# Kernel tuning notes

Measured on AMD Instinct MI355X. Metric: run time of the kernel, lower is better.

## Reference

```python
import jax, jax.numpy as jnp
import numpy as np
import math

B, H, S, D = 8, 16, 256, 256  # S == D is required by the module's math

def setup_inputs() -> dict:
    key = jax.random.key(0)
    kq, kk, kv, km = jax.random.split(key, 4)
    q = jax.random.normal(kq, (B, H, S, D), dtype=jnp.float32)
    k = jax.random.normal(kk, (B, H, S, D), dtype=jnp.float32)
    v = jax.random.normal(kv, (B, H, S, D), dtype=jnp.float32)
    u = jax.random.uniform(km, (1, H, S, S), dtype=jnp.float32)
    # additive mask: large negative where 'masked', 0.0 elsewhere
    mask = jnp.where(u > 0.7, jnp.float32(-1000.0), jnp.float32(0.0))
    return {"q": q, "k": k, "v": v, "mask": mask}

def reference(q, k, v, mask):
    scale = 1.0 / math.sqrt(q.shape[-1])
    # qk: [B,H,S,S]
    qk = jnp.einsum('bhsd,bhtd->bhst', q, k) * scale + mask
    # first matmul with v: [B,H,S,D] (D == S)
    attn = jnp.einsum('bhst,bhtd->bhsd', qk, v)
    # masked_fill where additive mask == 0.0 (broadcasts [1,H,S,S] -> [B,H,S,D])
    attn = jnp.where(mask == 0.0, jnp.float32(-1e9), attn)
    attn = jax.nn.softmax(attn.astype(jnp.float32), axis=-1).astype(q.dtype)
    # second matmul with v: [B,H,S,D]
    out = jnp.einsum('bhst,bhtd->bhsd', attn, v)
    return out
```

## Files before the change

kernel.cpp:

```cpp
#include <hip/hip_runtime.h>
#include <math.h>

namespace {
constexpr int S  = 256;
constexpr int NT = 256;
constexpr float SCALE = 0.0625f;
constexpr int KLD = 264;
}

typedef __bf16 bf16x4 __attribute__((ext_vector_type(4)));
typedef __bf16 bf16x8 __attribute__((ext_vector_type(8)));
typedef float  f32x4  __attribute__((ext_vector_type(4)));

#define MFMA(a, b, c) __builtin_amdgcn_mfma_f32_16x16x32_bf16((a), (b), (c), 0, 0, 0)

__global__ __launch_bounds__(NT) void vsplit_kernel(
    const float* __restrict__ v,
    __bf16* __restrict__ vth, __bf16* __restrict__ vtl, __bf16* __restrict__ vtll)
{
    __shared__ float tile[32][257];
    const int bh = blockIdx.x >> 3;
    const int tc = blockIdx.x & 7;
    const int tid = threadIdx.x;

    const float* vb = v + (size_t)bh * S * S + (size_t)tc * 32 * S;
    {
        const int c4 = (tid & 63) * 4;
        const int r  = tid >> 6;
        #pragma unroll
        for (int rr = 0; rr < 8; ++rr) {
            const int row = rr * 4 + r;
            const float4 f = *(const float4*)&vb[(size_t)row * S + c4];
            tile[row][c4 + 0] = f.x; tile[row][c4 + 1] = f.y;
            tile[row][c4 + 2] = f.z; tile[row][c4 + 3] = f.w;
        }
    }
    __syncthreads();

    const size_t obase = (size_t)bh * S * S + (size_t)tc * 8192;
    #pragma unroll
    for (int it = 0; it < 4; ++it) {
        const int id  = it * 256 + tid;
        const int j   = id >> 6;
        const int l4  = (id >> 4) & 3;
        const int l15 = id & 15;
        const int d   = j * 16 + l15;
        const int t0  = l4 * 8;
        bf16x8 hv, lv, llv;
        #pragma unroll
        for (int e = 0; e < 8; ++e) {
            const float x = tile[t0 + e][d];
            const __bf16 hi = (__bf16)x;
            const float  hf = (float)hi;
            const __bf16 lo = (__bf16)(x - hf);
            const float  lf = (float)lo;
            hv[e] = hi; lv[e] = lo; llv[e] = (__bf16)(x - hf - lf);
        }
        const size_t oi = obase + (size_t)id * 8;
        *(bf16x8*)&vth[oi]  = hv;
        *(bf16x8*)&vtl[oi]  = lv;
        *(bf16x8*)&vtll[oi] = llv;
    }
}

__global__ __launch_bounds__(NT, 2) void qkt_kernel(
    const float* __restrict__ q, const float* __restrict__ k,
    __bf16* __restrict__ r_hi, __bf16* __restrict__ r_lo, int swz)
{
    __shared__ __align__(16) __bf16 kh[64 * KLD];
    __shared__ __align__(16) __bf16 kl[64 * KLD];

    const int tid = threadIdx.x;
    const int w = tid >> 6, l = tid & 63, l15 = l & 15, l4 = l >> 4;

    int L = blockIdx.x;
    if (swz) L = (blockIdx.x & 7) * ((int)gridDim.x >> 3) + (blockIdx.x >> 3);
    const int bh = L >> 4;
    const int s0 = ((L >> 2) & 3) << 6;
    const int t0 = (L & 3) << 6;

    const float* qb = q + ((size_t)bh << 16);
    const float* kb = k + ((size_t)bh << 16);

    {
        const float* ksrc = kb + (size_t)t0 * S;
        #pragma unroll 4
        for (int it = 0; it < 16; ++it) {
            const int idx = it * 1024 + tid * 4;
            const float4 f = *(const float4*)&ksrc[idx];
            const float xs[4] = {f.x, f.y, f.z, f.w};
            bf16x4 hv, lv;
            #pragma unroll
            for (int e = 0; e < 4; ++e) {
                const __bf16 hi = (__bf16)xs[e];
                hv[e] = hi; lv[e] = (__bf16)(xs[e] - (float)hi);
            }
            const int row = idx >> 8;
            const int col = idx & 255;
            *(bf16x4*)&kh[row * KLD + col] = hv;
            *(bf16x4*)&kl[row * KLD + col] = lv;
        }
    }

    bf16x8 qh[8], ql[8];
    {
        const float* qr = qb + (size_t)(s0 + 16 * w + l15) * S;
        #pragma unroll
        for (int kc = 0; kc < 8; ++kc) {
            const float4 f0 = *(const float4*)&qr[kc * 32 + l4 * 8];
            const float4 f1 = *(const float4*)&qr[kc * 32 + l4 * 8 + 4];
            const float xs[8] = {f0.x, f0.y, f0.z, f0.w, f1.x, f1.y, f1.z, f1.w};
            bf16x8 hv, lv;
            #pragma unroll
            for (int e = 0; e < 8; ++e) {
                const float x = xs[e] * SCALE;
                const __bf16 hi = (__bf16)x;
                hv[e] = hi; lv[e] = (__bf16)(x - (float)hi);
            }
            qh[kc] = hv; ql[kc] = lv;
        }
    }
    __syncthreads();

    f32x4 acc[4];
    #pragma unroll
    for (int j = 0; j < 4; ++j) acc[j] = (f32x4){0.f, 0.f, 0.f, 0.f};

    #pragma unroll
    for (int kc = 0; kc < 8; ++kc) {
        #pragma unroll
        for (int j = 0; j < 4; ++j) {
            const int bo = (j * 16 + l15) * KLD + kc * 32 + l4 * 8;
            const bf16x8 khf = *(const bf16x8*)&kh[bo];
            const bf16x8 klf = *(const bf16x8*)&kl[bo];
            acc[j] = MFMA(qh[kc], khf, acc[j]);
            acc[j] = MFMA(qh[kc], klf, acc[j]);
            acc[j] = MFMA(ql[kc], khf, acc[j]);
        }
    }

    __bf16* rh_b = r_hi + ((size_t)bh << 16);
    __bf16* rl_b = r_lo + ((size_t)bh << 16);
    #pragma unroll
    for (int j = 0; j < 4; ++j) {
        #pragma unroll
        for (int rr = 0; rr < 4; ++rr) {
            const int row = s0 + 16 * w + l4 * 4 + rr;
            const int t   = t0 + j * 16 + l15;
            const float rv = acc[j][rr];
            const __bf16 hi = (__bf16)rv;
            rh_b[(size_t)row * S + t] = hi;
            rl_b[(size_t)row * S + t] = (__bf16)(rv - (float)hi);
        }
    }
}

#define SRC_OF(sp) ((sp) == 0 ? vth : (sp) == 1 ? vtl : vtll)

#define P2_LOAD(tc)                                                           \
    _Pragma("unroll")                                                         \
    for (int r_ = 0; r_ < 12; ++r_) {                                         \
        const int sp_ = r_ >> 2, qt_ = r_ & 3;                                \
        const __bf16* s_ = SRC_OF(sp_);                                       \
        stg[r_] = *(const bf16x8*)&s_[hb + (size_t)(tc) * 8192 + qt_ * 2048 + tid * 8]; \
    }

#define P2_WRITE()                                                            \
    _Pragma("unroll")                                                         \
    for (int r_ = 0; r_ < 12; ++r_) {                                         \
        const int sp_ = r_ >> 2, qt_ = r_ & 3;                                \
        *(bf16x8*)&arena[sp_ * 8192 + qt_ * 2048 + tid * 8] = stg[r_];        \
    }

#define P3_LOAD(tc)                                                           \
    _Pragma("unroll")                                                         \
    for (int r_ = 0; r_ < 8; ++r_) {                                          \
        const int sp_ = r_ >> 2, qt_ = r_ & 3;                                \
        const __bf16* s_ = SRC_OF(sp_);                                       \
        stg[r_] = *(const bf16x8*)&s_[hb + (size_t)(tc) * 8192 + qt_ * 2048 + tid * 8]; \
    }

#define P3_WRITE()                                                            \
    _Pragma("unroll")                                                         \
    for (int r_ = 0; r_ < 8; ++r_) {                                          \
        const int sp_ = r_ >> 2, qt_ = r_ & 3;                                \
        *(bf16x8*)&arena[16384 + sp_ * 8192 + qt_ * 2048 + tid * 8] = stg[r_];\
    }

__global__ __launch_bounds__(NT, 2) void attn2_kernel(
    const float* __restrict__ mask,
    const __bf16* __restrict__ r_hi, const __bf16* __restrict__ r_lo,
    const __bf16* __restrict__ vth, const __bf16* __restrict__ vtl,
    const __bf16* __restrict__ vtll,
    float* __restrict__ out, int H, int swz)
{
    __shared__ __align__(16) __bf16 arena[32768];

    const int tid = threadIdx.x;
    const int w = tid >> 6, l = tid & 63, l15 = l & 15, l4 = l >> 4;

    int L = blockIdx.x;
    if (swz) L = (blockIdx.x & 7) * ((int)gridDim.x >> 3) + (blockIdx.x >> 3);
    const int bh = L >> 2;
    const int s0 = (L & 3) << 6;
    const int h  = bh % H;

    const size_t hb = (size_t)bh << 16;
    const float* mbase = mask + ((size_t)h << 16);

    const int arow_g = s0 + 16 * w + l15;
    const __bf16* rh_p = r_hi + hb + (size_t)arow_g * S;
    const __bf16* rl_p = r_lo + hb + (size_t)arow_g * S;
    const float*  m_p  = mbase + (size_t)arow_g * S;

    bf16x8 stg[12];

    f32x4 acc2[16];
    #pragma unroll
    for (int j = 0; j < 16; ++j) acc2[j] = (f32x4){0.f, 0.f, 0.f, 0.f};

    P2_LOAD(0);
    P2_WRITE();
    P2_LOAD(1);
    bf16x8 rhc, rlc; float4 m0c, m1c;
    {
        const int ko_ = l4 * 8;
        rhc = *(const bf16x8*)&rh_p[ko_];
        rlc = *(const bf16x8*)&rl_p[ko_];
        m0c = *(const float4*)&m_p[ko_];
        m1c = *(const float4*)&m_p[ko_ + 4];
    }
    __syncthreads();

    #pragma unroll
    for (int tc = 0; tc < 8; ++tc) {
        bf16x8 rhn, rln; float4 m0n, m1n;
        if (tc < 7) {
            const int ko_ = (tc + 1) * 32 + l4 * 8;
            rhn = *(const bf16x8*)&rh_p[ko_];
            rln = *(const bf16x8*)&rl_p[ko_];
            m0n = *(const float4*)&m_p[ko_];
            m1n = *(const float4*)&m_p[ko_ + 4];
        }
        bf16x8 mf;
        mf[0] = (__bf16)m0c.x; mf[1] = (__bf16)m0c.y;
        mf[2] = (__bf16)m0c.z; mf[3] = (__bf16)m0c.w;
        mf[4] = (__bf16)m1c.x; mf[5] = (__bf16)m1c.y;
        mf[6] = (__bf16)m1c.z; mf[7] = (__bf16)m1c.w;

        #pragma unroll
        for (int j = 0; j < 16; ++j) {
            const int fo = j * 512 + l * 8;
            const bf16x8 vh  = *(const bf16x8*)&arena[fo];
            const bf16x8 vl  = *(const bf16x8*)&arena[8192 + fo];
            const bf16x8 vll = *(const bf16x8*)&arena[16384 + fo];
            acc2[j] = MFMA(mf,  vh,  acc2[j]);
            acc2[j] = MFMA(mf,  vl,  acc2[j]);
            acc2[j] = MFMA(mf,  vll, acc2[j]);
            acc2[j] = MFMA(rhc, vh,  acc2[j]);
            acc2[j] = MFMA(rhc, vl,  acc2[j]);
            acc2[j] = MFMA(rlc, vh,  acc2[j]);
        }
        __syncthreads();
        if (tc < 7) {
            P2_WRITE();
            if (tc < 6) P2_LOAD(tc + 2);
            rhc = rhn; rlc = rln; m0c = m0n; m1c = m1n;
            __syncthreads();
        }
    }

    P3_LOAD(0);

    #pragma unroll
    for (int rr = 0; rr < 4; ++rr) {
        const int srow = 16 * w + l4 * 4 + rr;
        const float* mrow = mbase + (size_t)(s0 + srow) * S;
        float mx = -3.4e38f;
        #pragma unroll
        for (int j = 0; j < 16; ++j) {
            const float mval = mrow[j * 16 + l15];
            const float a = (mval == 0.0f) ? -1e9f : acc2[j][rr];
            acc2[j][rr] = a;
            mx = fmaxf(mx, a);
        }
        #pragma unroll
        for (int off = 1; off < 16; off <<= 1)
            mx = fmaxf(mx, __shfl_xor(mx, off, 64));
        float sm = 0.f;
        #pragma unroll
        for (int j = 0; j < 16; ++j) {
            const float e = __expf(acc2[j][rr] - mx);
            acc2[j][rr] = e;
            sm += e;
        }
        #pragma unroll
        for (int off = 1; off < 16; off <<= 1)
            sm += __shfl_xor(sm, off, 64);
        const float inv = 1.0f / sm;
        #pragma unroll
        for (int j = 0; j < 16; ++j) {
            const int t = j * 16 + l15;
            arena[((srow << 8) + t) ^ ((srow & 7) << 3)] = (__bf16)(acc2[j][rr] * inv);
        }
    }
    P3_WRITE();
    P3_LOAD(1);
    __syncthreads();

    f32x4 acc3[16];
    #pragma unroll
    for (int j = 0; j < 16; ++j) acc3[j] = (f32x4){0.f, 0.f, 0.f, 0.f};

    const int prow = 16 * w + l15;
    #pragma unroll
    for (int tc = 0; tc < 8; ++tc) {
        const int pb = ((prow << 8) + tc * 32 + l4 * 8) ^ ((prow & 7) << 3);
        const bf16x8 pa = *(const bf16x8*)&arena[pb];
        #pragma unroll
        for (int j = 0; j < 16; ++j) {
            const int fo = 16384 + j * 512 + l * 8;
            acc3[j] = MFMA(pa, *(const bf16x8*)&arena[fo], acc3[j]);
            acc3[j] = MFMA(pa, *(const bf16x8*)&arena[8192 + fo], acc3[j]);
        }
        __syncthreads();
        if (tc < 7) {
            P3_WRITE();
            if (tc < 6) P3_LOAD(tc + 2);
            __syncthreads();
        }
    }

    float* ob = out + hb + (size_t)s0 * S;
    #pragma unroll
    for (int j = 0; j < 16; ++j) {
        #pragma unroll
        for (int rr = 0; rr < 4; ++rr)
            ob[(size_t)(16 * w + l4 * 4 + rr) * S + j * 16 + l15] = acc3[j][rr];
    }
}

__global__ __launch_bounds__(NT) void transpose_k_kernel(
    const float* __restrict__ k, float* __restrict__ kt)
{
    __shared__ float tile[64][65];
    const int tileIdx = blockIdx.x & 15;
    const int bh      = blockIdx.x >> 4;
    const int ti = (tileIdx >> 2) * 64;
    const int tj = (tileIdx & 3) * 64;
    const float* kb = k  + (size_t)bh * S * S;
    float*      ktb = kt + (size_t)bh * S * S;
    const int c  = threadIdx.x & 63;
    const int r4 = threadIdx.x >> 6;
    #pragma unroll
    for (int rr = 0; rr < 64; rr += 4)
        tile[rr + r4][c] = kb[(size_t)(ti + rr + r4) * S + tj + c];
    __syncthreads();
    #pragma unroll
    for (int rr = 0; rr < 64; rr += 4)
        ktb[(size_t)(tj + rr + r4) * S + ti + c] = tile[c][rr + r4];
}

template <int RPB>
__global__ __launch_bounds__(NT) void fused_attn_rpb(
    const float* __restrict__ q, const float* __restrict__ kt,
    const float* __restrict__ v, const float* __restrict__ mask,
    float* __restrict__ out, int nbh, int H, int swizzle)
{
    __shared__ float qT[S][RPB];
    __shared__ float sT[S][RPB];
    __shared__ float redbuf[4][RPB];

    const int tid = threadIdx.x;
    constexpr int NRB = S / RPB;
    int bh, rb;
    if (swizzle) {
        const int xcd  = blockIdx.x & 7;
        const int slot = blockIdx.x >> 3;
        const int hpx  = nbh >> 3;
        bh = xcd * hpx + (slot % hpx);
        rb = slot / hpx;
    } else {
        bh = blockIdx.x / NRB;
        rb = blockIdx.x % NRB;
    }
    const int h  = bh % H;
    const int s0 = rb * RPB;

    const float* qb  = q    + (size_t)bh * S * S;
    const float* ktb = kt   + (size_t)bh * S * S;
    const float* vb  = v    + (size_t)bh * S * S;
    const float* mb  = mask + (size_t)h  * S * S + (size_t)s0 * S;
    float*       ob  = out  + (size_t)bh * S * S + (size_t)s0 * S;

    #pragma unroll
    for (int si = 0; si < RPB; ++si)
        qT[tid][si] = qb[(size_t)(s0 + si) * S + tid];
    __syncthreads();

    {
        float acc[RPB];
        #pragma unroll
        for (int si = 0; si < RPB; ++si) acc[si] = 0.f;
        #pragma unroll 4
        for (int i = 0; i < S; ++i) {
            const float kv = ktb[(size_t)i * S + tid];
            #pragma unroll
            for (int si4 = 0; si4 < RPB; si4 += 4) {
                const float4 qa = *reinterpret_cast<const float4*>(&qT[i][si4]);
                acc[si4+0] = fmaf(qa.x, kv, acc[si4+0]);
                acc[si4+1] = fmaf(qa.y, kv, acc[si4+1]);
                acc[si4+2] = fmaf(qa.z, kv, acc[si4+2]);
                acc[si4+3] = fmaf(qa.w, kv, acc[si4+3]);
            }
        }
        #pragma unroll
        for (int si4 = 0; si4 < RPB; si4 += 4) {
            float4 t4;
            t4.x = fmaf(acc[si4+0], SCALE, mb[(size_t)(si4+0)*S + tid]);
            t4.y = fmaf(acc[si4+1], SCALE, mb[(size_t)(si4+1)*S + tid]);
            t4.z = fmaf(acc[si4+2], SCALE, mb[(size_t)(si4+2)*S + tid]);
            t4.w = fmaf(acc[si4+3], SCALE, mb[(size_t)(si4+3)*S + tid]);
            *reinterpret_cast<float4*>(&sT[tid][si4]) = t4;
        }
    }
    __syncthreads();

    float a1[RPB];
    #pragma unroll
    for (int si = 0; si < RPB; ++si) a1[si] = 0.f;
    #pragma unroll 2
    for (int t = 0; t < S; ++t) {
        const float vv = vb[(size_t)t * S + tid];
        #pragma unroll
        for (int si4 = 0; si4 < RPB; si4 += 4) {
            const float4 pa = *reinterpret_cast<const float4*>(&sT[t][si4]);
            a1[si4+0] = fmaf(pa.x, vv, a1[si4+0]);
            a1[si4+1] = fmaf(pa.y, vv, a1[si4+1]);
            a1[si4+2] = fmaf(pa.z, vv, a1[si4+2]);
            a1[si4+3] = fmaf(pa.w, vv, a1[si4+3]);
        }
    }
    #pragma unroll
    for (int si = 0; si < RPB; ++si)
        if (mb[(size_t)si * S + tid] == 0.0f) a1[si] = -1e9f;

    const int lane = tid & 63;
    const int wv   = tid >> 6;
    #pragma unroll
    for (int si = 0; si < RPB; ++si) {
        float m = a1[si];
        #pragma unroll
        for (int off = 32; off > 0; off >>= 1)
            m = fmaxf(m, __shfl_down(m, off, 64));
        if (lane == 0) redbuf[wv][si] = m;
    }
    __syncthreads();
    float e[RPB];
    #pragma unroll
    for (int si = 0; si < RPB; ++si) {
        const float m = fmaxf(fmaxf(redbuf[0][si], redbuf[1][si]),
                              fmaxf(redbuf[2][si], redbuf[3][si]));
        e[si] = __expf(a1[si] - m);
    }
    __syncthreads();
    #pragma unroll
    for (int si = 0; si < RPB; ++si) {
        float sm = e[si];
        #pragma unroll
        for (int off = 32; off > 0; off >>= 1)
            sm += __shfl_down(sm, off, 64);
        if (lane == 0) redbuf[wv][si] = sm;
    }
    __syncthreads();
    #pragma unroll
    for (int si4 = 0; si4 < RPB; si4 += 4) {
        float4 t4;
        #pragma unroll
        for (int jj = 0; jj < 4; ++jj) {
            const int si = si4 + jj;
            const float sm = redbuf[0][si] + redbuf[1][si] +
                             redbuf[2][si] + redbuf[3][si];
            (&t4.x)[jj] = e[si] / sm;
        }
        *reinterpret_cast<float4*>(&sT[tid][si4]) = t4;
    }
    __syncthreads();

    float o[RPB];
    #pragma unroll
    for (int si = 0; si < RPB; ++si) o[si] = 0.f;
    #pragma unroll 2
    for (int t = 0; t < S; ++t) {
        const float vv = vb[(size_t)t * S + tid];
        #pragma unroll
        for (int si4 = 0; si4 < RPB; si4 += 4) {
            const float4 pa = *reinterpret_cast<const float4*>(&sT[t][si4]);
            o[si4+0] = fmaf(pa.x, vv, o[si4+0]);
            o[si4+1] = fmaf(pa.y, vv, o[si4+1]);
            o[si4+2] = fmaf(pa.z, vv, o[si4+2]);
            o[si4+3] = fmaf(pa.w, vv, o[si4+3]);
        }
    }
    #pragma unroll
    for (int si = 0; si < RPB; ++si)
        ob[(size_t)si * S + tid] = o[si];
}

extern "C" void kernel_launch(void* const* d_in, const int* in_sizes, int n_in,
                              void* d_out, int out_size, void* d_ws, size_t ws_size,
                              hipStream_t stream) {
    const float* q    = (const float*)d_in[0];
    const float* k    = (const float*)d_in[1];
    const float* v    = (const float*)d_in[2];
    const float* mask = (const float*)d_in[3];
    float* out = (float*)d_out;

    const int nbh = in_sizes[0] / (S * S);
    const int H   = in_sizes[3] / (S * S);
    const size_t he = (size_t)nbh * S * S;
    const size_t need = he * sizeof(__bf16) * 5;
    const size_t kt_bytes = he * sizeof(float);

    if (ws_size >= need) {
        __bf16* vth  = (__bf16*)d_ws;
        __bf16* vtl  = vth + he;
        __bf16* vtll = vtl + he;
        __bf16* rhi  = vtll + he;
        __bf16* rlo  = rhi + he;
        const int nblk_q = nbh * 16;
        const int nblk_a = nbh * 4;
        const int swzq = (nblk_q % 8 == 0) ? 1 : 0;
        const int swza = (nblk_a % 8 == 0) ? 1 : 0;
        vsplit_kernel<<<dim3(nbh * 8), NT, 0, stream>>>(v, vth, vtl, vtll);
        qkt_kernel<<<dim3(nblk_q), NT, 0, stream>>>(q, k, rhi, rlo, swzq);
        attn2_kernel<<<dim3(nblk_a), NT, 0, stream>>>(
            mask, rhi, rlo, vth, vtl, vtll, out, H, swza);
    } else if (ws_size >= kt_bytes) {
        float* kt = (float*)d_ws;
        transpose_k_kernel<<<dim3(nbh * 16), NT, 0, stream>>>(k, kt);
        constexpr int RPB = 16;
        const int grid = nbh * (S / RPB);
        const int swz = (nbh % 8 == 0) ? 1 : 0;
        fused_attn_rpb<RPB><<<dim3(grid), NT, 0, stream>>>(
            q, kt, v, mask, out, nbh, H, swz);
    }
}
```

Measured before the change: 91.85 us.

## Merge V split and QK^T kernels into one launch; raise MFMA wave priority

The separate V-splitting kernel and QK^T kernel are combined into a single prep kernel whose blocks take one of three roles (two QK^T tiles, one V split tile) and share one LDS arena. This removes a kernel launch and the serialization gap between two independent passes, letting them overlap on the GPU. Separately, s_setprio is raised around the MFMA inner loops in the attention kernel to favour matrix issue over other waves. The merged kernel uses the larger LDS footprint for all blocks, which may reduce occupancy for the V role.

```diff
diff --git a/kernel.cpp b/kernel.cpp
--- a/kernel.cpp
+++ b/kernel.cpp
@@ -14,143 +14,152 @@
 
 #define MFMA(a, b, c) __builtin_amdgcn_mfma_f32_16x16x32_bf16((a), (b), (c), 0, 0, 0)
 
-__global__ __launch_bounds__(NT) void vsplit_kernel(
+__global__ __launch_bounds__(NT, 2) void prep_kernel(
+    const float* __restrict__ q, const float* __restrict__ k,
     const float* __restrict__ v,
-    __bf16* __restrict__ vth, __bf16* __restrict__ vtl, __bf16* __restrict__ vtll)
+    __bf16* __restrict__ vth, __bf16* __restrict__ vtl, __bf16* __restrict__ vtll,
+    __bf16* __restrict__ r_hi, __bf16* __restrict__ r_lo,
+    int nbh, int swzq)
 {
-    __shared__ float tile[32][257];
-    const int bh = blockIdx.x >> 3;
-    const int tc = blockIdx.x & 7;
-    const int tid = threadIdx.x;
-
-    const float* vb = v + (size_t)bh * S * S + (size_t)tc * 32 * S;
-    {
-        const int c4 = (tid & 63) * 4;
-        const int r  = tid >> 6;
-        #pragma unroll
-        for (int rr = 0; rr < 8; ++rr) {
-            const int row = rr * 4 + r;
-            const float4 f = *(const float4*)&vb[(size_t)row * S + c4];
-            tile[row][c4 + 0] = f.x; tile[row][c4 + 1] = f.y;
-            tile[row][c4 + 2] = f.z; tile[row][c4 + 3] = f.w;
-        }
-    }
-    __syncthreads();
-
-    const size_t obase = (size_t)bh * S * S + (size_t)tc * 8192;
-    #pragma unroll
-    for (int it = 0; it < 4; ++it) {
-        const int id  = it * 256 + tid;
-        const int j   = id >> 6;
-        const int l4  = (id >> 4) & 3;
-        const int l15 = id & 15;
-        const int d   = j * 16 + l15;
-        const int t0  = l4 * 8;
-        bf16x8 hv, lv, llv;
-        #pragma unroll
-        for (int e = 0; e < 8; ++e) {
-            const float x = tile[t0 + e][d];
-            const __bf16 hi = (__bf16)x;
-            const float  hf = (float)hi;
-            const __bf16 lo = (__bf16)(x - hf);
-            const float  lf = (float)lo;
-            hv[e] = hi; lv[e] = lo; llv[e] = (__bf16)(x - hf - lf);
-        }
-        const size_t oi = obase + (size_t)id * 8;
-        *(bf16x8*)&vth[oi]  = hv;
-        *(bf16x8*)&vtl[oi]  = lv;
-        *(bf16x8*)&vtll[oi] = llv;
-    }
-}
-
-__global__ __launch_bounds__(NT, 2) void qkt_kernel(
-    const float* __restrict__ q, const float* __restrict__ k,
-    __bf16* __restrict__ r_hi, __bf16* __restrict__ r_lo, int swz)
-{
-    __shared__ __align__(16) __bf16 kh[64 * KLD];
-    __shared__ __align__(16) __bf16 kl[64 * KLD];
-
-    const int tid = threadIdx.x;
-    const int w = tid >> 6, l = tid & 63, l15 = l & 15, l4 = l >> 4;
-
-    int L = blockIdx.x;
-    if (swz) L = (blockIdx.x & 7) * ((int)gridDim.x >> 3) + (blockIdx.x >> 3);
-    const int bh = L >> 4;
-    const int s0 = ((L >> 2) & 3) << 6;
-    const int t0 = (L & 3) << 6;
-
-    const float* qb = q + ((size_t)bh << 16);
-    const float* kb = k + ((size_t)bh << 16);
-
-    {
-        const float* ksrc = kb + (size_t)t0 * S;
-        #pragma unroll 4
-        for (int it = 0; it < 16; ++it) {
-            const int idx = it * 1024 + tid * 4;
-            const float4 f = *(const float4*)&ksrc[idx];
-            const float xs[4] = {f.x, f.y, f.z, f.w};
-            bf16x4 hv, lv;
+    __shared__ __align__(16) unsigned char lds_arena[64 * KLD * 2 * 2];
+
+    const int tid  = threadIdx.x;
+    const int trio = blockIdx.x / 3;
+    const int role = blockIdx.x % 3;
+
+    if (role < 2) {
+        __bf16* kh = (__bf16*)lds_arena;
+        __bf16* kl = kh + 64 * KLD;
+
+        const int w = tid >> 6, l = tid & 63, l15 = l & 15, l4 = l >> 4;
+
+        int L = trio * 2 + role;
+        if (swzq) {
+            const int n = nbh * 16;
+            L = (L & 7) * (n >> 3) + (L >> 3);
+        }
+        const int bh = L >> 4;
+        const int s0 = ((L >> 2) & 3) << 6;
+        const int t0 = (L & 3) << 6;
+
+        const float* qb = q + ((size_t)bh << 16);
+        const float* kb = k + ((size_t)bh << 16);
+
+        {
+            const float* ksrc = kb + (size_t)t0 * S;
+            #pragma unroll 4
+            for (int it = 0; it < 16; ++it) {
+                const int idx = it * 1024 + tid * 4;
+                const float4 f = *(const float4*)&ksrc[idx];
+                const float xs[4] = {f.x, f.y, f.z, f.w};
+                bf16x4 hv, lv;
+                #pragma unroll
+                for (int e = 0; e < 4; ++e) {
+                    const __bf16 hi = (__bf16)xs[e];
+                    hv[e] = hi; lv[e] = (__bf16)(xs[e] - (float)hi);
+                }
+                const int row = idx >> 8;
+                const int col = idx & 255;
+                *(bf16x4*)&kh[row * KLD + col] = hv;
+                *(bf16x4*)&kl[row * KLD + col] = lv;
+            }
+        }
+
+        bf16x8 qh[8], ql[8];
+        {
+            const float* qr = qb + (size_t)(s0 + 16 * w + l15) * S;
             #pragma unroll
-            for (int e = 0; e < 4; ++e) {
-                const __bf16 hi = (__bf16)xs[e];
-                hv[e] = hi; lv[e] = (__bf16)(xs[e] - (float)hi);
-            }
-            const int row = idx >> 8;
-            const int col = idx & 255;
-            *(bf16x4*)&kh[row * KLD + col] = hv;
-            *(bf16x4*)&kl[row * KLD + col] = lv;
-        }
-    }
-
-    bf16x8 qh[8], ql[8];
-    {
-        const float* qr = qb + (size_t)(s0 + 16 * w + l15) * S;
+            for (int kc = 0; kc < 8; ++kc) {
+                const float4 f0 = *(const float4*)&qr[kc * 32 + l4 * 8];
+                const float4 f1 = *(const float4*)&qr[kc * 32 + l4 * 8 + 4];
+                const float xs[8] = {f0.x, f0.y, f0.z, f0.w, f1.x, f1.y, f1.z, f1.w};
+                bf16x8 hv, lv;
+                #pragma unroll
+                for (int e = 0; e < 8; ++e) {
+                    const float x = xs[e] * SCALE;
+                    const __bf16 hi = (__bf16)x;
+                    hv[e] = hi; lv[e] = (__bf16)(x - (float)hi);
+                }
+                qh[kc] = hv; ql[kc] = lv;
+            }
+        }
+        __syncthreads();
+
+        f32x4 acc[4];
+        #pragma unroll
+        for (int j = 0; j < 4; ++j) acc[j] = (f32x4){0.f, 0.f, 0.f, 0.f};
+
         #pragma unroll
         for (int kc = 0; kc < 8; ++kc) {
-            const float4 f0 = *(const float4*)&qr[kc * 32 + l4 * 8];
-            const float4 f1 = *(const float4*)&qr[kc * 32 + l4 * 8 + 4];
-            const float xs[8] = {f0.x, f0.y, f0.z, f0.w, f1.x, f1.y, f1.z, f1.w};
-            bf16x8 hv, lv;
+            #pragma unroll
+            for (int j = 0; j < 4; ++j) {
+                const int bo = (j * 16 + l15) * KLD + kc * 32 + l4 * 8;
+                const bf16x8 khf = *(const bf16x8*)&kh[bo];
+                const bf16x8 klf = *(const bf16x8*)&kl[bo];
+                acc[j] = MFMA(qh[kc], khf, acc[j]);
+                acc[j] = MFMA(qh[kc], klf, acc[j]);
+                acc[j] = MFMA(ql[kc], khf, acc[j]);
+            }
+        }
+
+        __bf16* rh_b = r_hi + ((size_t)bh << 16);
+        __bf16* rl_b = r_lo + ((size_t)bh << 16);
+        #pragma unroll
+        for (int j = 0; j < 4; ++j) {
+            #pragma unroll
+            for (int rr = 0; rr < 4; ++rr) {
+                const int row = s0 + 16 * w + l4 * 4 + rr;
+                const int t   = t0 + j * 16 + l15;
+                const float rv = acc[j][rr];
+                const __bf16 hi = (__bf16)rv;
+                rh_b[(size_t)row * S + t] = hi;
+                rl_b[(size_t)row * S + t] = (__bf16)(rv - (float)hi);
+            }
+        }
+    } else {
+        float (*tile)[257] = (float(*)[257])lds_arena;
+
+        const int vi = trio;
+        const int bh = vi >> 3;
+        const int tc = vi & 7;
+
+        const float* vb = v + (size_t)bh * S * S + (size_t)tc * 32 * S;
+        {
+            const int c4 = (tid & 63) * 4;
+            const int r  = tid >> 6;
+            #pragma unroll
+            for (int rr = 0; rr < 8; ++rr) {
+                const int row = rr * 4 + r;
+                const float4 f = *(const float4*)&vb[(size_t)row * S + c4];
+                tile[row][c4 + 0] = f.x; tile[row][c4 + 1] = f.y;
+                tile[row][c4 + 2] = f.z; tile[row][c4 + 3] = f.w;
+            }
+        }
+        __syncthreads();
+
+        const size_t obase = (size_t)bh * S * S + (size_t)tc * 8192;
+        #pragma unroll
+        for (int it = 0; it < 4; ++it) {
+            const int id  = it * 256 + tid;
+            const int j   = id >> 6;
+            const int l4  = (id >> 4) & 3;
+            const int l15 = id & 15;
+            const int d   = j * 16 + l15;
+            const int t0  = l4 * 8;
+            bf16x8 hv, lv, llv;
             #pragma unroll
             for (int e = 0; e < 8; ++e) {
-                const float x = xs[e] * SCALE;
+                const float x = tile[t0 + e][d];
                 const __bf16 hi = (__bf16)x;
-                hv[e] = hi; lv[e] = (__bf16)(x - (float)hi);
-            }
-            qh[kc] = hv; ql[kc] = lv;
-        }
-    }
-    __syncthreads();
-
-    f32x4 acc[4];
-    #pragma unroll
-    for (int j = 0; j < 4; ++j) acc[j] = (f32x4){0.f, 0.f, 0.f, 0.f};
-
-    #pragma unroll
-    for (int kc = 0; kc < 8; ++kc) {
-        #pragma unroll
-        for (int j = 0; j < 4; ++j) {
-            const int bo = (j * 16 + l15) * KLD + kc * 32 + l4 * 8;
-            const bf16x8 khf = *(const bf16x8*)&kh[bo];
-            const bf16x8 klf = *(const bf16x8*)&kl[bo];
-            acc[j] = MFMA(qh[kc], khf, acc[j]);
-            acc[j] = MFMA(qh[kc], klf, acc[j]);
-            acc[j] = MFMA(ql[kc], khf, acc[j]);
-        }
-    }
-
-    __bf16* rh_b = r_hi + ((size_t)bh << 16);
-    __bf16* rl_b = r_lo + ((size_t)bh << 16);
-    #pragma unroll
-    for (int j = 0; j < 4; ++j) {
-        #pragma unroll
-        for (int rr = 0; rr < 4; ++rr) {
-            const int row = s0 + 16 * w + l4 * 4 + rr;
-            const int t   = t0 + j * 16 + l15;
-            const float rv = acc[j][rr];
-            const __bf16 hi = (__bf16)rv;
-            rh_b[(size_t)row * S + t] = hi;
-            rl_b[(size_t)row * S + t] = (__bf16)(rv - (float)hi);
+                const float  hf = (float)hi;
+                const __bf16 lo = (__bf16)(x - hf);
+                const float  lf = (float)lo;
+                hv[e] = hi; lv[e] = lo; llv[e] = (__bf16)(x - hf - lf);
+            }
+            const size_t oi = obase + (size_t)id * 8;
+            *(bf16x8*)&vth[oi]  = hv;
+            *(bf16x8*)&vtl[oi]  = lv;
+            *(bf16x8*)&vtll[oi] = llv;
         }
     }
 }
@@ -248,6 +257,7 @@
         mf[4] = (__bf16)m1c.x; mf[5] = (__bf16)m1c.y;
         mf[6] = (__bf16)m1c.z; mf[7] = (__bf16)m1c.w;
 
+        __builtin_amdgcn_s_setprio(1);
         #pragma unroll
         for (int j = 0; j < 16; ++j) {
             const int fo = j * 512 + l * 8;
@@ -261,6 +271,7 @@
             acc2[j] = MFMA(rhc, vl,  acc2[j]);
             acc2[j] = MFMA(rlc, vh,  acc2[j]);
         }
+        __builtin_amdgcn_s_setprio(0);
         __syncthreads();
         if (tc < 7) {
             P2_WRITE();
@@ -317,12 +328,14 @@
     for (int tc = 0; tc < 8; ++tc) {
         const int pb = ((prow << 8) + tc * 32 + l4 * 8) ^ ((prow & 7) << 3);
         const bf16x8 pa = *(const bf16x8*)&arena[pb];
+        __builtin_amdgcn_s_setprio(1);
         #pragma unroll
         for (int j = 0; j < 16; ++j) {
             const int fo = 16384 + j * 512 + l * 8;
             acc3[j] = MFMA(pa, *(const bf16x8*)&arena[fo], acc3[j]);
             acc3[j] = MFMA(pa, *(const bf16x8*)&arena[8192 + fo], acc3[j]);
         }
+        __builtin_amdgcn_s_setprio(0);
         __syncthreads();
         if (tc < 7) {
             P3_WRITE();
@@ -532,8 +545,8 @@
         const int nblk_a = nbh * 4;
         const int swzq = (nblk_q % 8 == 0) ? 1 : 0;
         const int swza = (nblk_a % 8 == 0) ? 1 : 0;
-        vsplit_kernel<<<dim3(nbh * 8), NT, 0, stream>>>(v, vth, vtl, vtll);
-        qkt_kernel<<<dim3(nblk_q), NT, 0, stream>>>(q, k, rhi, rlo, swzq);
+        prep_kernel<<<dim3(nbh * 24), NT, 0, stream>>>(
+            q, k, v, vth, vtl, vtll, rhi, rlo, nbh, swzq);
         attn2_kernel<<<dim3(nblk_a), NT, 0, stream>>>(
             mask, rhi, rlo, vth, vtl, vtll, out, H, swza);
     } else if (ws_size >= kt_bytes) {
```

New measurement: 85.73 us. -6.7%, faster.

## Store QK result in MFMA-fragment layout via LDS staging; raise priority around MFMAs

Applied to the files above, without the earlier changes.

The first kernel now stages its split hi/lo QK results through shared memory and writes them to global memory in a blocked, MFMA-fragment-ordered layout with 16-byte vector stores, instead of scattered 2-byte stores. The main kernel reads those fragments with contiguous per-lane vector loads rather than strided row loads. This targets uncoalesced global write and read traffic on the intermediate. It also wraps the MFMA loops in s_setprio so waves doing matrix math get scheduling priority, at the cost of an extra LDS round trip and a barrier in the producer kernel.

```diff
diff --git a/kernel.cpp b/kernel.cpp
--- a/kernel.cpp
+++ b/kernel.cpp
@@ -138,20 +138,34 @@
             acc[j] = MFMA(ql[kc], khf, acc[j]);
         }
     }
-
-    __bf16* rh_b = r_hi + ((size_t)bh << 16);
-    __bf16* rl_b = r_lo + ((size_t)bh << 16);
+    __syncthreads();
+
+    __bf16* rb = kh + w * 2048;
     #pragma unroll
     for (int j = 0; j < 4; ++j) {
+        const int tcgl = j >> 1;
+        const int jj   = j & 1;
         #pragma unroll
         for (int rr = 0; rr < 4; ++rr) {
-            const int row = s0 + 16 * w + l4 * 4 + rr;
-            const int t   = t0 + j * 16 + l15;
             const float rv = acc[j][rr];
             const __bf16 hi = (__bf16)rv;
-            rh_b[(size_t)row * S + t] = hi;
-            rl_b[(size_t)row * S + t] = (__bf16)(rv - (float)hi);
-        }
+            const __bf16 lo = (__bf16)(rv - (float)hi);
+            const int elem = ((l4 * 4 + rr) + 16 * (2 * jj + (l15 >> 3))) * 8
+                           + (l15 & 7);
+            rb[tcgl * 1024 + elem]       = hi;
+            rb[tcgl * 1024 + 512 + elem] = lo;
+        }
+    }
+    const int sb = (s0 >> 4) + w;
+    const size_t hb = (size_t)bh << 16;
+    #pragma unroll
+    for (int tcgl = 0; tcgl < 2; ++tcgl) {
+        const bf16x8 ph = *(const bf16x8*)&rb[tcgl * 1024 + l * 8];
+        const bf16x8 pl = *(const bf16x8*)&rb[tcgl * 1024 + 512 + l * 8];
+        const size_t oi = hb + (size_t)sb * 4096
+                        + (size_t)((t0 >> 5) + tcgl) * 512 + l * 8;
+        *(bf16x8*)&r_hi[oi] = ph;
+        *(bf16x8*)&r_lo[oi] = pl;
     }
 }
 
@@ -208,10 +222,10 @@
     const size_t hb = (size_t)bh << 16;
     const float* mbase = mask + ((size_t)h << 16);
 
-    const int arow_g = s0 + 16 * w + l15;
-    const __bf16* rh_p = r_hi + hb + (size_t)arow_g * S;
-    const __bf16* rl_p = r_lo + hb + (size_t)arow_g * S;
-    const float*  m_p  = mbase + (size_t)arow_g * S;
+    const int sb_a = (s0 >> 4) + w;
+    const __bf16* rh_p = r_hi + hb + (size_t)sb_a * 4096;
+    const __bf16* rl_p = r_lo + hb + (size_t)sb_a * 4096;
+    const float*  m_p  = mbase + (size_t)(s0 + 16 * w + l15) * S;
 
     bf16x8 stg[12];
 
@@ -224,11 +238,10 @@
     P2_LOAD(1);
     bf16x8 rhc, rlc; float4 m0c, m1c;
     {
-        const int ko_ = l4 * 8;
-        rhc = *(const bf16x8*)&rh_p[ko_];
-        rlc = *(const bf16x8*)&rl_p[ko_];
-        m0c = *(const float4*)&m_p[ko_];
-        m1c = *(const float4*)&m_p[ko_ + 4];
+        rhc = *(const bf16x8*)&rh_p[l * 8];
+        rlc = *(const bf16x8*)&rl_p[l * 8];
+        m0c = *(const float4*)&m_p[l4 * 8];
+        m1c = *(const float4*)&m_p[l4 * 8 + 4];
     }
     __syncthreads();
 
@@ -236,9 +249,9 @@
     for (int tc = 0; tc < 8; ++tc) {
         bf16x8 rhn, rln; float4 m0n, m1n;
         if (tc < 7) {
+            rhn = *(const bf16x8*)&rh_p[(tc + 1) * 512 + l * 8];
+            rln = *(const bf16x8*)&rl_p[(tc + 1) * 512 + l * 8];
             const int ko_ = (tc + 1) * 32 + l4 * 8;
-            rhn = *(const bf16x8*)&rh_p[ko_];
-            rln = *(const bf16x8*)&rl_p[ko_];
             m0n = *(const float4*)&m_p[ko_];
             m1n = *(const float4*)&m_p[ko_ + 4];
         }
@@ -248,6 +261,7 @@
         mf[4] = (__bf16)m1c.x; mf[5] = (__bf16)m1c.y;
         mf[6] = (__bf16)m1c.z; mf[7] = (__bf16)m1c.w;
 
+        __builtin_amdgcn_s_setprio(1);
         #pragma unroll
         for (int j = 0; j < 16; ++j) {
             const int fo = j * 512 + l * 8;
@@ -261,6 +275,7 @@
             acc2[j] = MFMA(rhc, vl,  acc2[j]);
             acc2[j] = MFMA(rlc, vh,  acc2[j]);
         }
+        __builtin_amdgcn_s_setprio(0);
         __syncthreads();
         if (tc < 7) {
             P2_WRITE();
@@ -317,12 +332,14 @@
     for (int tc = 0; tc < 8; ++tc) {
         const int pb = ((prow << 8) + tc * 32 + l4 * 8) ^ ((prow & 7) << 3);
         const bf16x8 pa = *(const bf16x8*)&arena[pb];
+        __builtin_amdgcn_s_setprio(1);
         #pragma unroll
         for (int j = 0; j < 16; ++j) {
             const int fo = 16384 + j * 512 + l * 8;
             acc3[j] = MFMA(pa, *(const bf16x8*)&arena[fo], acc3[j]);
             acc3[j] = MFMA(pa, *(const bf16x8*)&arena[8192 + fo], acc3[j]);
         }
+        __builtin_amdgcn_s_setprio(0);
         __syncthreads();
         if (tc < 7) {
             P3_WRITE();
```

Result: no change. 90.76 us (-1.2%).
